# Optimization experiments

Measured on AMD Instinct MI355X. Metric: run time of the kernel, lower is better.

The kernel has to match this reference:

```python
import jax, jax.numpy as jnp
import numpy as np

N = 200000      # query points
D_IN = 3        # coordinate dims
H = 256         # hidden features
L = 4           # hidden layers (between first and last Perceptron)
S = 8           # n_series == out_features


def setup_inputs() -> dict:
    key = jax.random.key(0)
    ks = jax.random.split(key, 7)
    coords = jax.random.normal(ks[0], (N, D_IN), dtype=jnp.float32)
    # Stacked per-series weights (all series share shapes; original loads the
    # same checkpoint into each, but we use independent random params).
    scale0 = 1.0 / np.sqrt(D_IN)
    scaleh = 1.0 / np.sqrt(H)
    W0 = jax.random.uniform(ks[1], (S, D_IN, H), jnp.float32, -scale0, scale0)
    b0 = jax.random.uniform(ks[2], (S, H), jnp.float32, -scale0, scale0)
    Wh = jax.random.uniform(ks[3], (S, L, H, H), jnp.float32, -scaleh, scaleh)
    bh = jax.random.uniform(ks[4], (S, L, H), jnp.float32, -scaleh, scaleh)
    Wout = jax.random.uniform(ks[5], (S, H, 1), jnp.float32, -scaleh, scaleh)
    bout = jax.random.uniform(ks[6], (S, 1), jnp.float32, -scaleh, scaleh)
    return {"coords": coords, "W0": W0, "b0": b0, "Wh": Wh, "bh": bh,
            "Wout": Wout, "bout": bout}


def reference(coords, W0, b0, Wh, bh, Wout, bout):
    # All S series' MLPs batched into grouped GEMMs (einsum over series axis s).
    # Perceptron = Linear + softplus; last layer is plain Linear.
    h = jax.nn.softplus(jnp.einsum('nd,sdh->snh', coords, W0) + b0[:, None, :])
    for i in range(L):  # small fixed layer count
        h = jax.nn.softplus(
            jnp.einsum('snh,shk->snk', h, Wh[:, i]) + bh[:, i][:, None, :])
    out = jnp.einsum('snh,sho->sno', h, Wout) + bout[:, None, :]  # [S,N,1]
    output = jnp.transpose(out[..., 0], (1, 0))  # concat along dim=1 -> [N,S]
    return (output, coords)
```

## Files before the change

kernel.cpp:

```cpp
#include <hip/hip_runtime.h>
#include <hip/hip_bf16.h>
#include <cstdint>

typedef __attribute__((ext_vector_type(8))) short short8;
typedef __attribute__((ext_vector_type(4))) float float4v;

#define LOG2E 1.44269504088896340736f
#define LN2   0.69314718055994530942f

#if __has_builtin(__builtin_amdgcn_exp2f)
__device__ __forceinline__ float fexp2(float x){ return __builtin_amdgcn_exp2f(x); }
#else
__device__ __forceinline__ float fexp2(float x){ return exp2f(x); }
#endif
#if __has_builtin(__builtin_amdgcn_logf)
__device__ __forceinline__ float flog2(float x){ return __builtin_amdgcn_logf(x); }
#else
__device__ __forceinline__ float flog2(float x){ return log2f(x); }
#endif

__device__ __forceinline__ float softplus_hat(float zh){
  return flog2(1.0f + fexp2(zh));
}

__device__ __forceinline__ unsigned short bf16_trunc(float f){
  return (unsigned short)(__builtin_bit_cast(unsigned int, f) >> 16);
}

#define HSTRIDE 264
#define MISTEP  4288
#define HSIZE   (64 * 264 + 16 * 16)

__global__ void convert_wh(const float* __restrict__ Wh,
                           unsigned short* __restrict__ Wt){
  int e = blockIdx.x * 256 + threadIdx.x;
  int n  = e & 255;
  int k  = (e >> 8) & 255;
  int sl = e >> 16;
  float v = Wh[e];
  __hip_bfloat16 h = __float2bfloat16(v);
  Wt[(sl << 16) + ((k >> 5) << 13) + (n << 5) + (k & 31)] =
      __builtin_bit_cast(unsigned short, h);
}

__device__ __forceinline__ float4v bf16_mfma(short8 a, short8 b, float4v c){
  return __builtin_amdgcn_mfma_f32_16x16x32_bf16(a, b, c, 0, 0, 0);
}

__device__ __forceinline__ void l0_rows(
    unsigned short* __restrict__ ht, const float4v* __restrict__ c4,
    int j, int c, float w0, float w1, float w2, float bb)
{
  float4v x0 = c4[j*3+0], x1 = c4[j*3+1], x2 = c4[j*3+2];
  float z0 = fmaf(x0.z, w2, fmaf(x0.y, w1, fmaf(x0.x, w0, bb)));
  float z1 = fmaf(x1.y, w2, fmaf(x1.x, w1, fmaf(x0.w, w0, bb)));
  float z2 = fmaf(x2.x, w2, fmaf(x1.w, w1, fmaf(x1.z, w0, bb)));
  float z3 = fmaf(x2.w, w2, fmaf(x2.z, w1, fmaf(x2.y, w0, bb)));
  ht[(4*j+0)*HSTRIDE + j*16 + c] = bf16_trunc(softplus_hat(z0));
  ht[(4*j+1)*HSTRIDE + j*16 + c] = bf16_trunc(softplus_hat(z1));
  ht[(4*j+2)*HSTRIDE + j*16 + c] = bf16_trunc(softplus_hat(z2));
  ht[(4*j+3)*HSTRIDE + j*16 + c] = bf16_trunc(softplus_hat(z3));
}

__device__ __forceinline__ void sp2s(const float4v (&acc)[4][4],
    unsigned short* __restrict__ cptr, int kb, int sub)
{
  const int idx = kb * 2 + (sub >> 1);
  const int mi = idx >> 2, ni = idx & 3;
  const int r0 = (sub & 1) * 2;
  float4v v = acc[mi][ni];
  #pragma unroll
  for (int r = r0; r < r0 + 2; ++r)
    cptr[mi * MISTEP + r * HSTRIDE + ni * 16] = bf16_trunc(softplus_hat(v[r]));
}

__device__ __forceinline__ void spdot2s(const float4v (&acc)[4][4],
    const float (&wv)[4], float (&p)[16], int kb, int sub)
{
  const int idx = kb * 2 + (sub >> 1);
  const int mi = idx >> 2, ni = idx & 3;
  const int r0 = (sub & 1) * 2;
  float4v v = acc[mi][ni];
  #pragma unroll
  for (int r = r0; r < r0 + 2; ++r)
    p[mi * 4 + r] = fmaf(softplus_hat(v[r]), wv[ni], p[mi * 4 + r]);
}

template<int PH, bool LOADN, class F>
__device__ __forceinline__ void mfma_phase(
    const unsigned short* __restrict__ bb,
    const unsigned short* __restrict__ bn,
    const unsigned short* __restrict__ aptr,
    short8 (&bq)[3][4], float4v (&acc)[4][4], F&& other)
{
  short8 a0[4], a1[4];
  #pragma unroll
  for (int mi = 0; mi < 4; ++mi)
    a0[mi] = *(const short8*)(aptr + mi * MISTEP);

  #pragma unroll
  for (int kb = 0; kb < 8; ++kb) {
    short8* cur = (kb & 1) ? a1 : a0;
    short8* nxt = (kb & 1) ? a0 : a1;
    const int slot = (8 * PH + kb) % 3;
    #pragma unroll
    for (int sub = 0; sub < 4; ++sub) {
      #pragma unroll
      for (int ni = 0; ni < 4; ++ni)
        acc[sub][ni] = bf16_mfma(cur[sub], bq[slot][ni], acc[sub][ni]);
      if (sub == 1 && kb < 7) {
        #pragma unroll
        for (int mi = 0; mi < 4; ++mi)
          nxt[mi] = *(const short8*)(aptr + (kb + 1) * 32 + mi * MISTEP);
      }
      if (sub == 3) {
        if (kb < 5) {
          #pragma unroll
          for (int ni = 0; ni < 4; ++ni)
            bq[slot][ni] = *(const short8*)(bb + (kb + 3) * 8192 + ni * 512);
        } else if (LOADN) {
          #pragma unroll
          for (int ni = 0; ni < 4; ++ni)
            bq[slot][ni] = *(const short8*)(bn + (kb - 5) * 8192 + ni * 512);
        }
      }
      __builtin_amdgcn_sched_barrier(0);
      other(kb, sub);
      __builtin_amdgcn_sched_barrier(0);
    }
  }
}

__global__ __launch_bounds__(256, 2) void series_mlp(
    const float* __restrict__ coords,
    const float* __restrict__ W0, const float* __restrict__ b0,
    const float* __restrict__ bh,
    const float* __restrict__ Wout, const float* __restrict__ bout,
    const unsigned short* __restrict__ Wt,
    float* __restrict__ out)
{
  __shared__ __align__(16) unsigned short h_lds[2 * HSIZE];
  __shared__ float cbuf[384];

  const int tid  = threadIdx.x;
  const int lane = tid & 63;
  const int wave = tid >> 6;
  const int s    = blockIdx.x & 7;
  const int m0   = (blockIdx.x >> 3) * 128;

  const int q    = lane >> 4;
  const int lr   = lane & 15;
  const int colb = (wave << 6) + lr;

  {
    int i1 = m0 * 3 + tid;
    int i2 = i1 + 256;
    cbuf[tid] = coords[i1 < 599999 ? i1 : 599999];
    if (tid < 128) cbuf[tid + 256] = coords[i2 < 599999 ? i2 : 599999];
  }

  const int c = tid;
  const float w0  = W0[(s * 3 + 0) * 256 + c] * LOG2E;
  const float w1  = W0[(s * 3 + 1) * 256 + c] * LOG2E;
  const float w2  = W0[(s * 3 + 2) * 256 + c] * LOG2E;
  const float bb0 = b0[s * 256 + c] * LOG2E;

  const unsigned short* bbase0 = Wt + ((s << 2) << 16) + (colb << 5) + (q << 3);
  short8 bq[3][4];
  #pragma unroll
  for (int i = 0; i < 3; ++i)
    #pragma unroll
    for (int ni = 0; ni < 4; ++ni)
      bq[i][ni] = *(const short8*)(bbase0 + i * 8192 + ni * 512);

  const unsigned short* aptrA = h_lds + lr * HSTRIDE + (lr >> 2) * 16 + (q << 3);
  const unsigned short* aptrB = aptrA + HSIZE;
  unsigned short* cptrA = h_lds + q * 1072 + colb;
  unsigned short* cptrB = cptrA + HSIZE;

  const float* bh_s = bh + (s << 10);
  const float4v* c4 = (const float4v*)cbuf;

  __syncthreads();
  #pragma unroll
  for (int j = 0; j < 16; ++j)
    l0_rows(h_lds, c4, j, c, w0, w1, w2, bb0);
  __syncthreads();

  float4v accA[4][4], accB[4][4];

#define INIT_ACC(ACC, LIDX)                                                   \
  {                                                                           \
    float bias[4];                                                            \
    _Pragma("unroll")                                                         \
    for (int ni = 0; ni < 4; ++ni)                                            \
      bias[ni] = bh_s[(LIDX) * 256 + colb + ni * 16] * LOG2E;                 \
    _Pragma("unroll")                                                         \
    for (int mi = 0; mi < 4; ++mi)                                            \
      _Pragma("unroll")                                                       \
      for (int ni = 0; ni < 4; ++ni)                                          \
        ACC[mi][ni] = (float4v){bias[ni], bias[ni], bias[ni], bias[ni]};      \
  }

  const unsigned short* B0 = bbase0;
  const unsigned short* B1 = bbase0 + 65536;
  const unsigned short* B2 = bbase0 + 2 * 65536;
  const unsigned short* B3 = bbase0 + 3 * 65536;

  INIT_ACC(accA, 0)
  mfma_phase<0, true>(B0, B0, aptrA, bq, accA, [&](int kb, int sub){
    if (sub == 0) l0_rows(h_lds + HSIZE, c4 + 48, 2 * kb + 0, c, w0, w1, w2, bb0);
    if (sub == 2) l0_rows(h_lds + HSIZE, c4 + 48, 2 * kb + 1, c, w0, w1, w2, bb0);
  });
  __syncthreads();

  INIT_ACC(accB, 0)
  mfma_phase<1, true>(B0, B1, aptrB, bq, accB,
      [&](int kb, int sub){ sp2s(accA, cptrA, kb, sub); });
  __syncthreads();

  INIT_ACC(accA, 1)
  mfma_phase<2, true>(B1, B1, aptrA, bq, accA,
      [&](int kb, int sub){ sp2s(accB, cptrB, kb, sub); });
  __syncthreads();

  INIT_ACC(accB, 1)
  mfma_phase<3, true>(B1, B2, aptrB, bq, accB,
      [&](int kb, int sub){ sp2s(accA, cptrA, kb, sub); });
  __syncthreads();

  INIT_ACC(accA, 2)
  mfma_phase<4, true>(B2, B2, aptrA, bq, accA,
      [&](int kb, int sub){ sp2s(accB, cptrB, kb, sub); });
  __syncthreads();

  INIT_ACC(accB, 2)
  mfma_phase<5, true>(B2, B3, aptrB, bq, accB,
      [&](int kb, int sub){ sp2s(accA, cptrA, kb, sub); });
  __syncthreads();

  INIT_ACC(accA, 3)
  mfma_phase<6, true>(B3, B3, aptrA, bq, accA,
      [&](int kb, int sub){ sp2s(accB, cptrB, kb, sub); });
  __syncthreads();

  INIT_ACC(accB, 3)
  float wv[4];
  #pragma unroll
  for (int ni = 0; ni < 4; ++ni)
    wv[ni] = Wout[(s << 8) + colb + ni * 16];
  float pA[16], pB[16];
  #pragma unroll
  for (int i = 0; i < 16; ++i) pA[i] = 0.f;
  mfma_phase<7, false>(B3, B3, aptrB, bq, accB,
      [&](int kb, int sub){ spdot2s(accA, wv, pA, kb, sub); });

  #pragma unroll
  for (int i = 0; i < 16; ++i) pB[i] = 0.f;
  #pragma unroll
  for (int kb = 0; kb < 8; ++kb)
    #pragma unroll
    for (int sub = 0; sub < 4; ++sub)
      spdot2s(accB, wv, pB, kb, sub);

  __syncthreads();
  float* redA = (float*)h_lds;
  float* redB = redA + 64 * 68;
  #pragma unroll
  for (int mi = 0; mi < 4; ++mi)
    #pragma unroll
    for (int r = 0; r < 4; ++r) {
      int row = mi * 16 + (q << 2) + r;
      redA[row * 68 + (wave << 4) + lr] = pA[mi * 4 + r];
      redB[row * 68 + (wave << 4) + lr] = pB[mi * 4 + r];
    }
  __syncthreads();

  if (tid < 128) {
    const int t = tid & 63;
    const float* red = (tid < 64) ? redA : redB;
    const float4v* rr = (const float4v*)&red[t * 68];
    float4v a = rr[0];
    #pragma unroll
    for (int i = 1; i < 16; ++i) {
      float4v b = rr[i];
      a.x += b.x; a.y += b.y; a.z += b.z; a.w += b.w;
    }
    float tot = (a.x + a.y) + (a.z + a.w);
    int row = m0 + ((tid >> 6) << 6) + t;
    if (row < 200000)
      out[row * 8 + s] = fmaf(LN2, tot, bout[s]);
  }
#undef INIT_ACC
}

__global__ __launch_bounds__(256) void series_mlp_slow(
    const float* __restrict__ coords,
    const float* __restrict__ W0, const float* __restrict__ b0,
    const float* __restrict__ Wh, const float* __restrict__ bh,
    const float* __restrict__ Wout, const float* __restrict__ bout,
    float* __restrict__ out)
{
  __shared__ float hh[64 * 256];
  __shared__ float cbuf[192];
  __shared__ float red[256];
  const int tid = threadIdx.x;
  const int s   = blockIdx.y;
  const int m0  = blockIdx.x * 64;

  if (tid < 192) cbuf[tid] = coords[m0 * 3 + tid];
  __syncthreads();
  {
    const float w0 = W0[(s * 3 + 0) * 256 + tid];
    const float w1 = W0[(s * 3 + 1) * 256 + tid];
    const float w2 = W0[(s * 3 + 2) * 256 + tid];
    const float bb = b0[s * 256 + tid];
    for (int m = 0; m < 64; ++m) {
      float z = fmaf(cbuf[m * 3 + 2], w2,
                fmaf(cbuf[m * 3 + 1], w1,
                fmaf(cbuf[m * 3 + 0], w0, bb)));
      hh[m * 256 + tid] = LN2 * softplus_hat(z * LOG2E);
    }
  }
  __syncthreads();

  for (int l = 0; l < 4; ++l) {
    const float* W = Wh + (((s << 2) + l) << 16);
    const float bb = bh[((s << 2) + l) * 256 + tid];
    float acc[64];
    #pragma unroll
    for (int m = 0; m < 64; ++m) acc[m] = bb;
    for (int kc = 0; kc < 64; ++kc) {
      float w0 = W[(kc * 4 + 0) * 256 + tid];
      float w1 = W[(kc * 4 + 1) * 256 + tid];
      float w2 = W[(kc * 4 + 2) * 256 + tid];
      float w3 = W[(kc * 4 + 3) * 256 + tid];
      #pragma unroll
      for (int m = 0; m < 64; ++m) {
        float4v hv = *(const float4v*)&hh[m * 256 + kc * 4];
        acc[m] = fmaf(hv.w, w3, fmaf(hv.z, w2,
                 fmaf(hv.y, w1, fmaf(hv.x, w0, acc[m]))));
      }
    }
    __syncthreads();
    #pragma unroll
    for (int m = 0; m < 64; ++m)
      hh[m * 256 + tid] = LN2 * softplus_hat(acc[m] * LOG2E);
    __syncthreads();
  }
  {
    const int m = tid >> 2, qq = tid & 3;
    const float* wv = Wout + (s << 8);
    float sum = 0.f;
    for (int i = 0; i < 16; ++i) {
      int kk = (qq << 6) + ((((tid & 15) + i) << 2) & 63);
      float4v hv = *(const float4v*)&hh[m * 256 + kk];
      sum += hv.x * wv[kk] + hv.y * wv[kk + 1] + hv.z * wv[kk + 2] + hv.w * wv[kk + 3];
    }
    red[tid] = sum;
    __syncthreads();
    if (tid < 64)
      out[(m0 + tid) * 8 + s] =
          red[tid * 4] + red[tid * 4 + 1] + red[tid * 4 + 2] + red[tid * 4 + 3] + bout[s];
  }
}

extern "C" void kernel_launch(void* const* d_in, const int* in_sizes, int n_in,
                              void* d_out, int out_size, void* d_ws, size_t ws_size,
                              hipStream_t stream) {
  const float* coords = (const float*)d_in[0];
  const float* W0     = (const float*)d_in[1];
  const float* b0     = (const float*)d_in[2];
  const float* Wh     = (const float*)d_in[3];
  const float* bh     = (const float*)d_in[4];
  const float* Wout   = (const float*)d_in[5];
  const float* bout   = (const float*)d_in[6];
  float* out = (float*)d_out;

  const size_t WT_BYTES = (size_t)8 * 4 * 256 * 256 * 2;
  if (ws_size >= WT_BYTES) {
    unsigned short* Wt = (unsigned short*)d_ws;
    convert_wh<<<8192, 256, 0, stream>>>(Wh, Wt);
    series_mlp<<<dim3(12504), dim3(256), 0, stream>>>(
        coords, W0, b0, bh, Wout, bout, Wt, out);
  } else {
    series_mlp_slow<<<dim3(3125, 8), dim3(256), 0, stream>>>(
        coords, W0, b0, Wh, bh, Wout, bout, out);
  }
  hipMemcpyAsync(out + (size_t)200000 * 8, coords,
                 (size_t)200000 * 3 * sizeof(float),
                 hipMemcpyDeviceToDevice, stream);
}
```

Baseline: 904.7 us.

## Swap MFMA operand order to write packed bf16 pairs and shuffle-reduce output

Swaps the A/B operands of the bf16 MFMA so each lane's accumulator holds consecutive hidden features rather than consecutive rows. Activations can then be written to LDS as packed 64-bit bf16 pairs instead of scattered 16-bit stores. Biases are staged in LDS once and read as float4. The final output dot product uses per-row partial sums, cross-lane shuffles and a much smaller LDS reduction. This cuts LDS store instructions and reduction traffic, at the cost of extra LDS for the biases and a different accumulator layout that has to match the A-operand read pattern.

```diff
diff --git a/kernel.cpp b/kernel.cpp
--- a/kernel.cpp
+++ b/kernel.cpp
@@ -4,6 +4,7 @@
 
 typedef __attribute__((ext_vector_type(8))) short short8;
 typedef __attribute__((ext_vector_type(4))) float float4v;
+typedef __attribute__((ext_vector_type(2))) unsigned int uint2v;
 
 #define LOG2E 1.44269504088896340736f
 #define LN2   0.69314718055994530942f
@@ -27,6 +28,12 @@
   return (unsigned short)(__builtin_bit_cast(unsigned int, f) >> 16);
 }
 
+__device__ __forceinline__ unsigned int bf16_pack2(float lo, float hi){
+  return __builtin_amdgcn_perm(__builtin_bit_cast(unsigned int, hi),
+                               __builtin_bit_cast(unsigned int, lo),
+                               0x07060302u);
+}
+
 #define HSTRIDE 264
 #define MISTEP  4288
 #define HSIZE   (64 * 264 + 16 * 16)
@@ -62,8 +69,24 @@
   ht[(4*j+3)*HSTRIDE + j*16 + c] = bf16_trunc(softplus_hat(z3));
 }
 
-__device__ __forceinline__ void sp2s(const float4v (&acc)[4][4],
-    unsigned short* __restrict__ cptr, int kb, int sub)
+__device__ __forceinline__ void spw2(const float4v (&acc)[4][4],
+    unsigned short* __restrict__ cw, unsigned int& uh, int kb, int sub)
+{
+  const int idx = kb * 2 + (sub >> 1);
+  const int mi = idx >> 2, ni = idx & 3;
+  float4v v = acc[mi][ni];
+  if (!(sub & 1)) {
+    uh = bf16_pack2(softplus_hat(v.x), softplus_hat(v.y));
+  } else {
+    uint2v dd;
+    dd.x = uh;
+    dd.y = bf16_pack2(softplus_hat(v.z), softplus_hat(v.w));
+    *(uint2v*)(cw + mi * MISTEP + ni * 16) = dd;
+  }
+}
+
+__device__ __forceinline__ void spdot2(const float4v (&acc)[4][4],
+    const float4v (&wv4)[4], float (&p)[4], int kb, int sub)
 {
   const int idx = kb * 2 + (sub >> 1);
   const int mi = idx >> 2, ni = idx & 3;
@@ -71,19 +94,7 @@
   float4v v = acc[mi][ni];
   #pragma unroll
   for (int r = r0; r < r0 + 2; ++r)
-    cptr[mi * MISTEP + r * HSTRIDE + ni * 16] = bf16_trunc(softplus_hat(v[r]));
-}
-
-__device__ __forceinline__ void spdot2s(const float4v (&acc)[4][4],
-    const float (&wv)[4], float (&p)[16], int kb, int sub)
-{
-  const int idx = kb * 2 + (sub >> 1);
-  const int mi = idx >> 2, ni = idx & 3;
-  const int r0 = (sub & 1) * 2;
-  float4v v = acc[mi][ni];
-  #pragma unroll
-  for (int r = r0; r < r0 + 2; ++r)
-    p[mi * 4 + r] = fmaf(softplus_hat(v[r]), wv[ni], p[mi * 4 + r]);
+    p[mi] = fmaf(softplus_hat(v[r]), wv4[ni][r], p[mi]);
 }
 
 template<int PH, bool LOADN, class F>
@@ -107,7 +118,7 @@
     for (int sub = 0; sub < 4; ++sub) {
       #pragma unroll
       for (int ni = 0; ni < 4; ++ni)
-        acc[sub][ni] = bf16_mfma(cur[sub], bq[slot][ni], acc[sub][ni]);
+        acc[sub][ni] = bf16_mfma(bq[slot][ni], cur[sub], acc[sub][ni]);
       if (sub == 1 && kb < 7) {
         #pragma unroll
         for (int mi = 0; mi < 4; ++mi)
@@ -141,6 +152,7 @@
 {
   __shared__ __align__(16) unsigned short h_lds[2 * HSIZE];
   __shared__ float cbuf[384];
+  __shared__ __align__(16) float bias_lds[1024];
 
   const int tid  = threadIdx.x;
   const int lane = tid & 63;
@@ -158,6 +170,12 @@
     cbuf[tid] = coords[i1 < 599999 ? i1 : 599999];
     if (tid < 128) cbuf[tid + 256] = coords[i2 < 599999 ? i2 : 599999];
   }
+  {
+    const float* bh_s = bh + (s << 10);
+    #pragma unroll
+    for (int l = 0; l < 4; ++l)
+      bias_lds[l * 256 + tid] = bh_s[l * 256 + tid] * LOG2E;
+  }
 
   const int c = tid;
   const float w0  = W0[(s * 3 + 0) * 256 + c] * LOG2E;
@@ -173,12 +191,18 @@
     for (int ni = 0; ni < 4; ++ni)
       bq[i][ni] = *(const short8*)(bbase0 + i * 8192 + ni * 512);
 
+  float4v wv4[4];
+  #pragma unroll
+  for (int ni = 0; ni < 4; ++ni)
+    wv4[ni] = *(const float4v*)(Wout + (s << 8) + (wave << 6) + ni * 16 +
+                                (q << 2));
+
   const unsigned short* aptrA = h_lds + lr * HSTRIDE + (lr >> 2) * 16 + (q << 3);
   const unsigned short* aptrB = aptrA + HSIZE;
-  unsigned short* cptrA = h_lds + q * 1072 + colb;
-  unsigned short* cptrB = cptrA + HSIZE;
-
-  const float* bh_s = bh + (s << 10);
+  unsigned short* cwA = h_lds + lr * HSTRIDE + (lr >> 2) * 16 + (wave << 6) +
+                        (q << 2);
+  unsigned short* cwB = cwA + HSIZE;
+
   const float4v* c4 = (const float4v*)cbuf;
 
   __syncthreads();
@@ -191,15 +215,16 @@
 
 #define INIT_ACC(ACC, LIDX)                                                   \
   {                                                                           \
-    float bias[4];                                                            \
+    float4v b4[4];                                                            \
     _Pragma("unroll")                                                         \
     for (int ni = 0; ni < 4; ++ni)                                            \
-      bias[ni] = bh_s[(LIDX) * 256 + colb + ni * 16] * LOG2E;                 \
+      b4[ni] = *(const float4v*)&bias_lds[(LIDX) * 256 + (wave << 6) +        \
+                                          ni * 16 + (q << 2)];                \
     _Pragma("unroll")                                                         \
     for (int mi = 0; mi < 4; ++mi)                                            \
       _Pragma("unroll")                                                       \
       for (int ni = 0; ni < 4; ++ni)                                          \
-        ACC[mi][ni] = (float4v){bias[ni], bias[ni], bias[ni], bias[ni]};      \
+        ACC[mi][ni] = b4[ni];                                                 \
   }
 
   const unsigned short* B0 = bbase0;
@@ -214,79 +239,73 @@
   });
   __syncthreads();
 
+  unsigned int uh;
+
   INIT_ACC(accB, 0)
   mfma_phase<1, true>(B0, B1, aptrB, bq, accB,
-      [&](int kb, int sub){ sp2s(accA, cptrA, kb, sub); });
+      [&](int kb, int sub){ spw2(accA, cwA, uh, kb, sub); });
   __syncthreads();
 
   INIT_ACC(accA, 1)
   mfma_phase<2, true>(B1, B1, aptrA, bq, accA,
-      [&](int kb, int sub){ sp2s(accB, cptrB, kb, sub); });
+      [&](int kb, int sub){ spw2(accB, cwB, uh, kb, sub); });
   __syncthreads();
 
   INIT_ACC(accB, 1)
   mfma_phase<3, true>(B1, B2, aptrB, bq, accB,
-      [&](int kb, int sub){ sp2s(accA, cptrA, kb, sub); });
+      [&](int kb, int sub){ spw2(accA, cwA, uh, kb, sub); });
   __syncthreads();
 
   INIT_ACC(accA, 2)
   mfma_phase<4, true>(B2, B2, aptrA, bq, accA,
-      [&](int kb, int sub){ sp2s(accB, cptrB, kb, sub); });
+      [&](int kb, int sub){ spw2(accB, cwB, uh, kb, sub); });
   __syncthreads();
 
   INIT_ACC(accB, 2)
   mfma_phase<5, true>(B2, B3, aptrB, bq, accB,
-      [&](int kb, int sub){ sp2s(accA, cptrA, kb, sub); });
+      [&](int kb, int sub){ spw2(accA, cwA, uh, kb, sub); });
   __syncthreads();
 
   INIT_ACC(accA, 3)
   mfma_phase<6, true>(B3, B3, aptrA, bq, accA,
-      [&](int kb, int sub){ sp2s(accB, cptrB, kb, sub); });
+      [&](int kb, int sub){ spw2(accB, cwB, uh, kb, sub); });
   __syncthreads();
 
   INIT_ACC(accB, 3)
-  float wv[4];
-  #pragma unroll
-  for (int ni = 0; ni < 4; ++ni)
-    wv[ni] = Wout[(s << 8) + colb + ni * 16];
-  float pA[16], pB[16];
-  #pragma unroll
-  for (int i = 0; i < 16; ++i) pA[i] = 0.f;
+  float pA[4] = {0.f, 0.f, 0.f, 0.f};
+  float pB[4] = {0.f, 0.f, 0.f, 0.f};
   mfma_phase<7, false>(B3, B3, aptrB, bq, accB,
-      [&](int kb, int sub){ spdot2s(accA, wv, pA, kb, sub); });
-
-  #pragma unroll
-  for (int i = 0; i < 16; ++i) pB[i] = 0.f;
+      [&](int kb, int sub){ spdot2(accA, wv4, pA, kb, sub); });
+
   #pragma unroll
   for (int kb = 0; kb < 8; ++kb)
     #pragma unroll
     for (int sub = 0; sub < 4; ++sub)
-      spdot2s(accB, wv, pB, kb, sub);
+      spdot2(accB, wv4, pB, kb, sub);
+
+  #pragma unroll
+  for (int mi = 0; mi < 4; ++mi) {
+    pA[mi] += __shfl_xor(pA[mi], 16); pA[mi] += __shfl_xor(pA[mi], 32);
+    pB[mi] += __shfl_xor(pB[mi], 16); pB[mi] += __shfl_xor(pB[mi], 32);
+  }
 
   __syncthreads();
   float* redA = (float*)h_lds;
-  float* redB = redA + 64 * 68;
-  #pragma unroll
-  for (int mi = 0; mi < 4; ++mi)
-    #pragma unroll
-    for (int r = 0; r < 4; ++r) {
-      int row = mi * 16 + (q << 2) + r;
-      redA[row * 68 + (wave << 4) + lr] = pA[mi * 4 + r];
-      redB[row * 68 + (wave << 4) + lr] = pB[mi * 4 + r];
+  float* redB = redA + 256;
+  if (lane < 16) {
+    #pragma unroll
+    for (int mi = 0; mi < 4; ++mi) {
+      redA[(mi * 16 + lr) * 4 + wave] = pA[mi];
+      redB[(mi * 16 + lr) * 4 + wave] = pB[mi];
     }
+  }
   __syncthreads();
 
   if (tid < 128) {
     const int t = tid & 63;
     const float* red = (tid < 64) ? redA : redB;
-    const float4v* rr = (const float4v*)&red[t * 68];
-    float4v a = rr[0];
-    #pragma unroll
-    for (int i = 1; i < 16; ++i) {
-      float4v b = rr[i];
-      a.x += b.x; a.y += b.y; a.z += b.z; a.w += b.w;
-    }
-    float tot = (a.x + a.y) + (a.z + a.w);
+    float4v r4 = ((const float4v*)red)[t];
+    float tot = (r4.x + r4.y) + (r4.z + r4.w);
     int row = m0 + ((tid >> 6) << 6) + t;
     if (row < 200000)
       out[row * 8 + s] = fmaf(LN2, tot, bout[s]);
```

Result: slower. 928.8 us (+2.7%).
